# Kernel optimization log

Measured on AMD Instinct MI355X. Metric: run time of the kernel, lower is better.

## Reference

```python
import jax, jax.numpy as jnp
import numpy as np

# Body-part joint index groups (NTU-25 layout), as in the torch module
TORSO = np.array([0, 1, 2, 3, 20])
LEFT_HAND = np.array([8, 9, 10, 11, 23, 24])
LEFT_LEG = np.array([16, 17, 18, 19])
RIGHT_HAND = np.array([4, 5, 6, 7, 21, 22])
RIGHT_LEG = np.array([12, 13, 14, 15])
GROUPS = [TORSO, LEFT_HAND, LEFT_LEG, RIGHT_HAND, RIGHT_LEG]

N, C, T, V = 64, 256, 64, 25
HID = C // 16


def setup_inputs() -> dict:
    key = jax.random.key(0)
    k = jax.random.split(key, 5)
    x = jax.random.normal(k[0], (N, C, T, V), dtype=jnp.float32)
    # 5 branch MLPs (1x1 convs == linear over channels), stacked on leading axis f
    W1s = jax.random.normal(k[1], (5, HID, C), dtype=jnp.float32) * (1.0 / np.sqrt(C))
    b1s = jax.random.normal(k[2], (5, HID), dtype=jnp.float32) * 0.01
    W2s = jax.random.normal(k[3], (5, C, HID), dtype=jnp.float32) * (1.0 / np.sqrt(HID))
    b2s = jax.random.normal(k[4], (5, C), dtype=jnp.float32) * 0.01
    return {"x": x, "W1s": W1s, "b1s": b1s, "W2s": W2s, "b2s": b2s}


def _branch_mlp(p, W1s, b1s, W2s, b2s):
    # p: [N, C] pooled features; apply all 5 branch MLPs at once -> [N, 5, C]
    h = jax.nn.relu(jnp.einsum("nc,fhc->nfh", p, W1s) + b1s[None])  # [N,5,HID]
    return jnp.einsum("nfh,fch->nfc", h, W2s) + b2s[None]  # [N,5,C]


def reference(x, W1s, b1s, W2s, b2s):
    torso = x[:, :, :, TORSO]  # [N,C,T,5]
    avg = jnp.mean(torso, axis=(2, 3))  # [N,C] (AdaptiveAvgPool2d(1))
    mx = jnp.max(torso, axis=(2, 3))  # [N,C] (AdaptiveMaxPool2d(1))
    gates = jax.nn.sigmoid(_branch_mlp(avg, W1s, b1s, W2s, b2s)
                           + _branch_mlp(mx, W1s, b1s, W2s, b2s))  # [N,5,C]
    parts = [x[:, :, :, idx] * gates[:, i][:, :, None, None]
             for i, idx in enumerate(GROUPS)]
    return jnp.concatenate(parts, axis=3)  # [N,C,T,25]
```

## Files before the change

### kernel.cpp

```cpp
#include <hip/hip_runtime.h>
#include <math.h>

#define NB   64
#define CC   256
#define TT   64
#define VV   25
#define HID  16
#define NG   5
#define TORSO_CNT 5

__constant__ int SRC_J[25] = {0,1,2,3,20,  8,9,10,11,23,24,  16,17,18,19,  4,5,6,7,21,22,  12,13,14,15};
__constant__ int GRP_J[25] = {0,0,0,0,0,   1,1,1,1,1,1,      2,2,2,2,      3,3,3,3,3,3,   4,4,4,4};

__global__ void pool_kernel(const float* __restrict__ x,
                            float* __restrict__ avg_out,
                            float* __restrict__ max_out) {
    const int wave = threadIdx.x >> 6;
    const int lane = threadIdx.x & 63;
    const int pair = blockIdx.x * 4 + wave;
    const long long base = (long long)pair * (TT * VV) + (long long)lane * VV;

    float v0 = x[base + 0];
    float v1 = x[base + 1];
    float v2 = x[base + 2];
    float v3 = x[base + 3];
    float v4 = x[base + 20];

    float s = v0 + v1 + v2 + v3 + v4;
    float m = fmaxf(fmaxf(fmaxf(v0, v1), fmaxf(v2, v3)), v4);

    #pragma unroll
    for (int off = 32; off >= 1; off >>= 1) {
        s += __shfl_xor(s, off, 64);
        m = fmaxf(m, __shfl_xor(m, off, 64));
    }
    if (lane == 0) {
        avg_out[pair] = s * (1.0f / (TT * TORSO_CNT));
        max_out[pair] = m;
    }
}

__global__ void gates_kernel(const float* __restrict__ avg_in,
                             const float* __restrict__ max_in,
                             const float* __restrict__ W1s,
                             const float* __restrict__ b1s,
                             const float* __restrict__ W2s,
                             const float* __restrict__ b2s,
                             float* __restrict__ gates) {
    __shared__ float sAvg[CC];
    __shared__ float sMax[CC];
    __shared__ float sHA[NG * HID];
    __shared__ float sHM[NG * HID];

    const int n = blockIdx.x;
    const int tid = threadIdx.x;

    sAvg[tid] = avg_in[n * CC + tid];
    sMax[tid] = max_in[n * CC + tid];
    __syncthreads();

    if (tid < 2 * NG * HID) {
        const int type = tid / (NG * HID);
        const int rem  = tid % (NG * HID);
        const float* p = type ? sMax : sAvg;
        const float* w = W1s + rem * CC;
        float h = b1s[rem];
        #pragma unroll 8
        for (int c = 0; c < CC; ++c) h += w[c] * p[c];
        h = fmaxf(h, 0.0f);
        if (type) sHM[rem] = h; else sHA[rem] = h;
    }
    __syncthreads();

    const int c = tid;
    #pragma unroll
    for (int f = 0; f < NG; ++f) {
        const float* w2 = W2s + (f * CC + c) * HID;
        float g = 2.0f * b2s[f * CC + c];
        #pragma unroll
        for (int j = 0; j < HID; ++j)
            g += w2[j] * (sHA[f * HID + j] + sHM[f * HID + j]);
        gates[(n * NG + f) * CC + c] = 1.0f / (1.0f + expf(-g));
    }
}

__global__ void apply_kernel(const float* __restrict__ x,
                             const float* __restrict__ gates,
                             float* __restrict__ out,
                             int total4) {
    const int tid = blockIdx.x * blockDim.x + threadIdx.x;
    if (tid >= total4) return;
    const int base = tid * 4;

    float r[4];
    #pragma unroll
    for (int k = 0; k < 4; ++k) {
        const int idx = base + k;
        const unsigned row = (unsigned)idx / VV;
        const int p = idx - (int)row * VV;
        const unsigned nc = row / TT;
        const int c = nc & (CC - 1);
        const int n = nc >> 8;
        const float g = gates[(n * NG + GRP_J[p]) * CC + c];
        r[k] = x[(long long)row * VV + SRC_J[p]] * g;
    }
    float4 v = make_float4(r[0], r[1], r[2], r[3]);
    *reinterpret_cast<float4*>(out + base) = v;
}

extern "C" void kernel_launch(void* const* d_in, const int* in_sizes, int n_in,
                              void* d_out, int out_size, void* d_ws, size_t ws_size,
                              hipStream_t stream) {
    const float* x   = (const float*)d_in[0];
    const float* W1s = (const float*)d_in[1];
    const float* b1s = (const float*)d_in[2];
    const float* W2s = (const float*)d_in[3];
    const float* b2s = (const float*)d_in[4];
    float* out = (float*)d_out;

    float* avg   = (float*)d_ws;
    float* mx    = avg + NB * CC;
    float* gates = mx + NB * CC;

    pool_kernel<<<(NB * CC) / 4, 256, 0, stream>>>(x, avg, mx);

    gates_kernel<<<NB, CC, 0, stream>>>(avg, mx, W1s, b1s, W2s, b2s, gates);

    const int total  = NB * CC * TT * VV;
    const int total4 = total / 4;
    apply_kernel<<<(total4 + 255) / 256, 256, 0, stream>>>(x, gates, out, total4);
}
```

Measured before the change: 258.3 us.

## Stage rows in LDS for coalesced float4 permute-apply and vectorized pooling

The apply kernel now loads four (n,c) rows of x into shared memory with coalesced float4 reads, then performs the joint permutation and gating from LDS using a packed lookup table. Before, it did scattered per-element global gathers. The pool kernel reads full rows as float4 and masks in the torso joints instead of doing strided scalar loads. The gates kernel is vectorized with float4. The trade-off is that pooling now reads five times more data, and apply needs an LDS round-trip and a block-wide barrier.

Measured after the change: 218.6 us. -15.3%, faster.

```diff
diff --git a/kernel.cpp b/kernel.cpp
--- a/kernel.cpp
+++ b/kernel.cpp
@@ -7,35 +7,52 @@
 #define VV   25
 #define HID  16
 #define NG   5
-#define TORSO_CNT 5
+#define ROWF 1600
+#define ROWF4 400
+#define PAIRS 4
 
-__constant__ int SRC_J[25] = {0,1,2,3,20,  8,9,10,11,23,24,  16,17,18,19,  4,5,6,7,21,22,  12,13,14,15};
-__constant__ int GRP_J[25] = {0,0,0,0,0,   1,1,1,1,1,1,      2,2,2,2,      3,3,3,3,3,3,   4,4,4,4};
+#define TORSO_MASK 0x10000Fu
 
-__global__ void pool_kernel(const float* __restrict__ x,
+__constant__ int PERM_LUT[25] = {
+    0|(0<<8), 1|(0<<8), 2|(0<<8), 3|(0<<8), 20|(0<<8),
+    8|(1<<8), 9|(1<<8), 10|(1<<8), 11|(1<<8), 23|(1<<8), 24|(1<<8),
+    16|(2<<8), 17|(2<<8), 18|(2<<8), 19|(2<<8),
+    4|(3<<8), 5|(3<<8), 6|(3<<8), 7|(3<<8), 21|(3<<8), 22|(3<<8),
+    12|(4<<8), 13|(4<<8), 14|(4<<8), 15|(4<<8)
+};
+
+__global__ void pool_kernel(const float4* __restrict__ x4,
                             float* __restrict__ avg_out,
                             float* __restrict__ max_out) {
     const int wave = threadIdx.x >> 6;
     const int lane = threadIdx.x & 63;
     const int pair = blockIdx.x * 4 + wave;
-    const long long base = (long long)pair * (TT * VV) + (long long)lane * VV;
+    const int base4 = pair * ROWF4;
 
-    float v0 = x[base + 0];
-    float v1 = x[base + 1];
-    float v2 = x[base + 2];
-    float v3 = x[base + 3];
-    float v4 = x[base + 20];
-
-    float s = v0 + v1 + v2 + v3 + v4;
-    float m = fmaxf(fmaxf(fmaxf(v0, v1), fmaxf(v2, v3)), v4);
-
+    float s = 0.0f;
+    float m = -3.4e38f;
+    for (int i = lane; i < ROWF4; i += 64) {
+        float4 v = x4[base4 + i];
+        const int e = 4 * i;
+        int j = e % 25;
+        float vals[4] = {v.x, v.y, v.z, v.w};
+        #pragma unroll
+        for (int k = 0; k < 4; ++k) {
+            int jj = j + k;
+            if (jj >= 25) jj -= 25;
+            if ((TORSO_MASK >> jj) & 1u) {
+                s += vals[k];
+                m = fmaxf(m, vals[k]);
+            }
+        }
+    }
     #pragma unroll
     for (int off = 32; off >= 1; off >>= 1) {
         s += __shfl_xor(s, off, 64);
         m = fmaxf(m, __shfl_xor(m, off, 64));
     }
     if (lane == 0) {
-        avg_out[pair] = s * (1.0f / (TT * TORSO_CNT));
+        avg_out[pair] = s * (1.0f / (TT * 5));
         max_out[pair] = m;
     }
 }
@@ -47,26 +64,29 @@
                              const float* __restrict__ W2s,
                              const float* __restrict__ b2s,
                              float* __restrict__ gates) {
-    __shared__ float sAvg[CC];
-    __shared__ float sMax[CC];
+    __shared__ float4 sAvg[CC / 4];
+    __shared__ float4 sMax[CC / 4];
     __shared__ float sHA[NG * HID];
     __shared__ float sHM[NG * HID];
 
     const int n = blockIdx.x;
     const int tid = threadIdx.x;
 
-    sAvg[tid] = avg_in[n * CC + tid];
-    sMax[tid] = max_in[n * CC + tid];
+    if (tid < 64)       sAvg[tid]      = reinterpret_cast<const float4*>(avg_in + n * CC)[tid];
+    else if (tid < 128) sMax[tid - 64] = reinterpret_cast<const float4*>(max_in + n * CC)[tid - 64];
     __syncthreads();
 
     if (tid < 2 * NG * HID) {
         const int type = tid / (NG * HID);
         const int rem  = tid % (NG * HID);
-        const float* p = type ? sMax : sAvg;
-        const float* w = W1s + rem * CC;
+        const float4* p = type ? sMax : sAvg;
+        const float4* w = reinterpret_cast<const float4*>(W1s + rem * CC);
         float h = b1s[rem];
         #pragma unroll 8
-        for (int c = 0; c < CC; ++c) h += w[c] * p[c];
+        for (int c4 = 0; c4 < CC / 4; ++c4) {
+            float4 a = w[c4], b = p[c4];
+            h += a.x * b.x + a.y * b.y + a.z * b.z + a.w * b.w;
+        }
         h = fmaxf(h, 0.0f);
         if (type) sHM[rem] = h; else sHA[rem] = h;
     }
@@ -75,37 +95,62 @@
     const int c = tid;
     #pragma unroll
     for (int f = 0; f < NG; ++f) {
-        const float* w2 = W2s + (f * CC + c) * HID;
+        const float4* w2 = reinterpret_cast<const float4*>(W2s + (f * CC + c) * HID);
         float g = 2.0f * b2s[f * CC + c];
         #pragma unroll
-        for (int j = 0; j < HID; ++j)
-            g += w2[j] * (sHA[f * HID + j] + sHM[f * HID + j]);
+        for (int j4 = 0; j4 < HID / 4; ++j4) {
+            float4 w = w2[j4];
+            const int jb = f * HID + j4 * 4;
+            g += w.x * (sHA[jb + 0] + sHM[jb + 0]);
+            g += w.y * (sHA[jb + 1] + sHM[jb + 1]);
+            g += w.z * (sHA[jb + 2] + sHM[jb + 2]);
+            g += w.w * (sHA[jb + 3] + sHM[jb + 3]);
+        }
         gates[(n * NG + f) * CC + c] = 1.0f / (1.0f + expf(-g));
     }
 }
 
-__global__ void apply_kernel(const float* __restrict__ x,
+__global__ void apply_kernel(const float4* __restrict__ x4,
                              const float* __restrict__ gates,
-                             float* __restrict__ out,
-                             int total4) {
-    const int tid = blockIdx.x * blockDim.x + threadIdx.x;
-    if (tid >= total4) return;
-    const int base = tid * 4;
+                             float4* __restrict__ out4) {
+    __shared__ float lds[PAIRS * ROWF];
+    __shared__ float sg[PAIRS * NG];
+    __shared__ int sLut[VV];
 
-    float r[4];
+    const int tid = threadIdx.x;
+    const int nc0 = blockIdx.x * PAIRS;
+    const int base4 = nc0 * ROWF4;
+
     #pragma unroll
-    for (int k = 0; k < 4; ++k) {
-        const int idx = base + k;
-        const unsigned row = (unsigned)idx / VV;
-        const int p = idx - (int)row * VV;
-        const unsigned nc = row / TT;
-        const int c = nc & (CC - 1);
-        const int n = nc >> 8;
-        const float g = gates[(n * NG + GRP_J[p]) * CC + c];
-        r[k] = x[(long long)row * VV + SRC_J[p]] * g;
+    for (int i = tid; i < PAIRS * ROWF4; i += 256) {
+        reinterpret_cast<float4*>(lds)[i] = x4[base4 + i];
     }
-    float4 v = make_float4(r[0], r[1], r[2], r[3]);
-    *reinterpret_cast<float4*>(out + base) = v;
+    if (tid < PAIRS * NG) {
+        const int q = tid / NG, f = tid % NG;
+        const int nc = nc0 + q;
+        sg[tid] = gates[((nc >> 8) * NG + f) * CC + (nc & (CC - 1))];
+    }
+    if (tid < VV) sLut[tid] = PERM_LUT[tid];
+    __syncthreads();
+
+    #pragma unroll
+    for (int i = tid; i < PAIRS * ROWF4; i += 256) {
+        const int q = i / ROWF4;
+        const int e0 = 4 * (i - q * ROWF4);
+        int row = e0 / 25;
+        int p   = e0 - row * 25;
+        const float* lrow = lds + q * ROWF;
+        const float* gq   = sg + q * NG;
+        float r[4];
+        #pragma unroll
+        for (int k = 0; k < 4; ++k) {
+            const int lut = sLut[p];
+            r[k] = lrow[row * 25 + (lut & 0xFF)] * gq[lut >> 8];
+            ++p;
+            if (p >= 25) { p = 0; ++row; }
+        }
+        out4[base4 + i] = make_float4(r[0], r[1], r[2], r[3]);
+    }
 }
 
 extern "C" void kernel_launch(void* const* d_in, const int* in_sizes, int n_in,
@@ -116,17 +161,16 @@
     const float* b1s = (const float*)d_in[2];
     const float* W2s = (const float*)d_in[3];
     const float* b2s = (const float*)d_in[4];
-    float* out = (float*)d_out;
 
     float* avg   = (float*)d_ws;
     float* mx    = avg + NB * CC;
     float* gates = mx + NB * CC;
 
-    pool_kernel<<<(NB * CC) / 4, 256, 0, stream>>>(x, avg, mx);
+    pool_kernel<<<(NB * CC) / 4, 256, 0, stream>>>(
+        (const float4*)x, avg, mx);
 
     gates_kernel<<<NB, CC, 0, stream>>>(avg, mx, W1s, b1s, W2s, b2s, gates);
 
-    const int total  = NB * CC * TT * VV;
-    const int total4 = total / 4;
-    apply_kernel<<<(total4 + 255) / 256, 256, 0, stream>>>(x, gates, out, total4);
+    apply_kernel<<<(NB * CC) / PAIRS, 256, 0, stream>>>(
+        (const float4*)x, gates, (float4*)d_out);
 }
```
